# Kernel tuning notes

Hardware: AMD Instinct MI355X
Metric: run time of the kernel (lower is better)

Reference implementation:

```python
import jax, jax.numpy as jnp
import numpy as np

B, D, E, C = 16384, 768, 124, 6  # batch, emb_dim, n_experts, n_classes


def _mlp(h, w1, b1, w2, b2):
    # timm Mlp: fc1 -> GELU(exact) -> fc2, hidden = in_features
    return jax.nn.gelu(h @ w1 + b1, approximate=False) @ w2 + b2


def setup_inputs() -> dict:
    key = jax.random.key(0)
    ks = jax.random.split(key, 14)
    s = 0.02
    inp = {
        "x": jax.random.normal(ks[0], (B, D), dtype=jnp.float32),
        # per-sample expert counts in [1, E]
        "n_experts": jax.random.randint(ks[1], (B,), 1, E + 1, dtype=jnp.int64 if jax.config.jax_enable_x64 else jnp.int32),
        # classifier Mlp: D -> D -> E*C
        "cls_w1": jax.random.normal(ks[2], (D, D), dtype=jnp.float32) * s,
        "cls_b1": jnp.zeros((D,), jnp.float32),
        "cls_w2": jax.random.normal(ks[3], (D, E * C), dtype=jnp.float32) * s,
        "cls_b2": jnp.zeros((E * C,), jnp.float32),
        # which_expert Mlp: D -> D -> E
        "we_w1": jax.random.normal(ks[4], (D, D), dtype=jnp.float32) * s,
        "we_b1": jnp.zeros((D,), jnp.float32),
        "we_w2": jax.random.normal(ks[5], (D, E), dtype=jnp.float32) * s,
        "we_b2": jnp.zeros((E,), jnp.float32),
        # expert_weights Mlp: D -> D -> E
        "ew_w1": jax.random.normal(ks[6], (D, D), dtype=jnp.float32) * s,
        "ew_b1": jnp.zeros((D,), jnp.float32),
        "ew_w2": jax.random.normal(ks[7], (D, E), dtype=jnp.float32) * s,
        "ew_b2": jnp.zeros((E,), jnp.float32),
    }
    return inp


def reference(x, n_experts, cls_w1, cls_b1, cls_w2, cls_b2,
              we_w1, we_b1, we_w2, we_b2, ew_w1, ew_b1, ew_w2, ew_b2):
    emb = x  # backbone = identity
    expert_logits = _mlp(emb, cls_w1, cls_b1, cls_w2, cls_b2).reshape(B, E, C)
    expert_weight_logits = _mlp(emb, ew_w1, ew_b1, ew_w2, ew_b2)  # [B, E]
    which_expert = _mlp(emb, we_w1, we_b1, we_w2, we_b2)          # [B, E]

    n = jnp.minimum(n_experts, E)                                  # clamp to n_experts
    # kth_largest: sort descending, pick (n-1)-th per row -> threshold
    sorted_desc = -jnp.sort(-which_expert, axis=1)
    threshold = sorted_desc[jnp.arange(B), n - 1][:, None]         # [B, 1]
    mask = which_expert < threshold

    expert_weight_logits = jnp.where(mask, -jnp.inf, expert_weight_logits)
    expert_proba = jax.nn.softmax(expert_logits, axis=2)           # over classes
    expert_weights = jax.nn.softmax(expert_weight_logits, axis=1)  # over experts

    combined = (expert_proba * expert_weights[:, :, None]).sum(axis=1)
    return combined / expert_weights.sum(axis=1)[:, None]          # [B, C]
```

## Files before the change

kernel.cpp:

```cpp
#include <hip/hip_runtime.h>
#include <stdint.h>

typedef unsigned short u16;
typedef short short8 __attribute__((ext_vector_type(8)));
typedef float f32x4 __attribute__((ext_vector_type(4)));

#define NB 16384

#define OFF_XHI      0ull
#define OFF_XLO      25165824ull
#define OFF_LCLS     0ull
#define OFF_LWE_P0   25165824ull
#define OFF_LWE_P1   33554432ull
#define OFF_LWE_P2   41943040ull
#define OFF_BT1      50331648ull
#define OFF_LEWB     50331648ull
#define OFF_BTWE_HI  52690944ull
#define OFF_BTWE_LO  53870592ull
#define OFF_BT2CLS   55050240ull
#define OFF_BT2EW    56229888ull
#define OFF_BT2WE_HI 56426496ull
#define OFF_BT2WE_LO 56623104ull
#define OFF_B1CE     56819712ull
#define OFF_B1WE     56825856ull
#define OFF_B2CLS    56828928ull
#define OFF_B2EW     56832000ull
#define OFF_B2WE     56832512ull
#define OFF_HCLSEW   56833024ull
#define OFF_HWE_HI   107164672ull
#define OFF_HWE_LO   132330496ull
#define WS_NEED      157496320ull

__device__ __forceinline__ u16 f2bf(float f) {
  uint32_t u = __float_as_uint(f);
  u += 0x7fffu + ((u >> 16) & 1u);
  return (u16)(u >> 16);
}
__device__ __forceinline__ float bf2f(u16 h) {
  return __uint_as_float(((uint32_t)h) << 16);
}
__device__ __forceinline__ void g2l16(const u16* g, u16* l) {
  __builtin_amdgcn_global_load_lds(
      (__attribute__((address_space(1))) void*)(u16*)g,
      (__attribute__((address_space(3))) void*)l, 16, 0, 0);
}

__global__ void prep_all(
    const float* __restrict__ x, u16* __restrict__ xhi, u16* __restrict__ xlo,
    const float* __restrict__ cls_w1, const float* __restrict__ ew_w1,
    const float* __restrict__ we_w1,  const float* __restrict__ cls_w2,
    const float* __restrict__ ew_w2,  const float* __restrict__ we_w2,
    u16* BT1, u16* BTwe_hi, u16* BTwe_lo,
    u16* BT2cls, u16* BT2ew, u16* BT2we_hi, u16* BT2we_lo,
    const float* __restrict__ cls_b1, const float* __restrict__ ew_b1,
    const float* __restrict__ we_b1,  const float* __restrict__ cls_b2,
    const float* __restrict__ ew_b2,  const float* __restrict__ we_b2,
    float* b1ce, float* b1we, float* b2cls, float* b2ew, float* b2we) {
  __shared__ float t[64][65];
  const int bid = blockIdx.x;
  if (bid < 12288) {
    int i = bid * 256 + threadIdx.x;
    float4 v = ((const float4*)x)[i];
    ushort4 h, l;
    h.x = f2bf(v.x); l.x = f2bf(v.x - bf2f(h.x));
    h.y = f2bf(v.y); l.y = f2bf(v.y - bf2f(h.y));
    h.z = f2bf(v.z); l.z = f2bf(v.z - bf2f(h.z));
    h.w = f2bf(v.w); l.w = f2bf(v.w - bf2f(h.w));
    ((ushort4*)xhi)[i] = h;
    ((ushort4*)xlo)[i] = l;
    return;
  }
  if (bid < 13152) {
    const int idx = bid - 12288;
    const int bx = idx % 12, by = (idx / 12) % 12, bz = idx / 144;
    const float* src; int N; u16* dhi; u16* dlo = nullptr;
    switch (bz) {
      case 0: src = cls_w1; N = 768; dhi = BT1; break;
      case 1: src = ew_w1;  N = 768; dhi = BT1 + 768 * 768; break;
      case 2: src = we_w1;  N = 768; dhi = BTwe_hi; dlo = BTwe_lo; break;
      case 3: src = cls_w2; N = 744; dhi = BT2cls; break;
      case 4: src = ew_w2;  N = 124; dhi = BT2ew; break;
      default: src = we_w2; N = 124; dhi = BT2we_hi; dlo = BT2we_lo; break;
    }
    const int Npad = (N + 127) & ~127;
    const int n0 = by * 64;
    if (n0 >= Npad) return;
    const int k0 = bx * 64;
    const int tx = threadIdx.x & 63, tg = threadIdx.x >> 6;
#pragma unroll
    for (int r = 0; r < 16; ++r) {
      int k = tg * 16 + r;
      int n = n0 + tx;
      t[k][tx] = (n < N) ? src[(size_t)(k0 + k) * N + n] : 0.f;
    }
    __syncthreads();
#pragma unroll
    for (int r = 0; r < 16; ++r) {
      int n = n0 + tg * 16 + r;
      if (n < Npad) {
        float v = t[tx][tg * 16 + r];
        u16 h = f2bf(v);
        dhi[(size_t)n * 768 + k0 + tx] = h;
        if (dlo) dlo[(size_t)n * 768 + k0 + tx] = f2bf(v - bf2f(h));
      }
    }
    return;
  }
  int id = (bid - 13152) * 256 + threadIdx.x;
  if (id < 1536) { b1ce[id] = (id < 768) ? cls_b1[id] : ew_b1[id - 768]; return; }
  id -= 1536;
  if (id < 768) { b1we[id] = we_b1[id]; return; }
  id -= 768;
  if (id < 768) { b2cls[id] = (id < 744) ? cls_b2[id] : 0.f; return; }
  id -= 768;
  if (id < 128) { b2ew[id] = (id < 124) ? ew_b2[id] : 0.f; return; }
  id -= 128;
  if (id < 128) { b2we[id] = (id < 124) ? we_b2[id] : 0.f; return; }
}

__device__ __forceinline__ void gemm_core(
    const u16* A0, const u16* A1, const u16* A2, int lda,
    const u16* B0, const u16* B1, const u16* B2,
    int npass, int K, int bm, int tid, u16* sA, u16* sB, f32x4 acc[4][4]) {
  const int lane = tid & 63;
  const int wv = tid >> 6;
  const int wr = wv >> 1, wc = wv & 1;
  const int sr = lane >> 3;
  const int sc = (((lane & 7) ^ sr) << 3);
  for (int p = 0; p < npass; ++p) {
    const u16* A = (p == 0) ? A0 : ((p == 1) ? A1 : A2);
    const u16* Bp = (p == 0) ? B0 : ((p == 1) ? B1 : B2);
    const u16* gA = A + (size_t)(bm + wv * 32 + sr) * lda + sc;
    const u16* gB = Bp + (size_t)(wv * 32 + sr) * K + sc;
    u16* lA = sA + (wv * 32) * 64;
    u16* lB = sB + (wv * 32) * 64;
    for (int kt = 0; kt < K; kt += 64) {
#pragma unroll
      for (int s = 0; s < 4; ++s) {
        g2l16(gA + (size_t)(s * 8) * lda + kt, lA + s * 8 * 64);
        g2l16(gB + (size_t)(s * 8) * K + kt, lB + s * 8 * 64);
      }
      __syncthreads();
#pragma unroll
      for (int ks = 0; ks < 2; ++ks) {
        const int co = ((ks * 4 + (lane >> 4)) ^ (lane & 7)) * 8;
        short8 av[4], bv[4];
#pragma unroll
        for (int i = 0; i < 4; i++)
          av[i] = *(const short8*)(sA + (wr * 64 + i * 16 + (lane & 15)) * 64 + co);
#pragma unroll
        for (int j = 0; j < 4; j++)
          bv[j] = *(const short8*)(sB + (wc * 64 + j * 16 + (lane & 15)) * 64 + co);
#pragma unroll
        for (int i = 0; i < 4; i++)
#pragma unroll
          for (int j = 0; j < 4; j++)
            acc[i][j] = __builtin_amdgcn_mfma_f32_16x16x32_bf16(av[i], bv[j], acc[i][j], 0, 0, 0);
      }
      __syncthreads();
    }
  }
}

__device__ __forceinline__ void gemm_split_core(
    const u16* __restrict__ Ahi, const u16* __restrict__ Alo, int lda,
    const u16* __restrict__ Bhi, const u16* __restrict__ Blo, int ldb,
    int K, int bm, int tid, u16* sA, u16* sB, f32x4 acc[4][4]) {
  const int lane = tid & 63;
  const int wv = tid >> 6;
  const int wr = wv >> 1, wc = wv & 1;
  const int sr = lane >> 3;
  const int gl = (lane & 7) ^ sr;
  const int koff = (gl & 3) << 3;
  const u16* Asel = (gl < 4) ? Ahi : Alo;
  const u16* Bsel = (gl < 4) ? Bhi : Blo;
  const u16* gA = Asel + (size_t)(bm + wv * 32 + sr) * lda + koff;
  const u16* gB = Bsel + (size_t)(wv * 32 + sr) * ldb + koff;
  u16* lA = sA + (wv * 32) * 64;
  u16* lB = sB + (wv * 32) * 64;

  for (int kt = 0; kt < K; kt += 32) {
#pragma unroll
    for (int s = 0; s < 4; ++s) {
      g2l16(gA + (size_t)(s * 8) * lda + kt, lA + s * 8 * 64);
      g2l16(gB + (size_t)(s * 8) * ldb + kt, lB + s * 8 * 64);
    }
    __syncthreads();
    const int coh = (((lane >> 4) ^ (lane & 7)) << 3);
    short8 ah[4], al[4], bh[4], bl[4];
#pragma unroll
    for (int i = 0; i < 4; i++) {
      const u16* p = sA + (wr * 64 + i * 16 + (lane & 15)) * 64;
      ah[i] = *(const short8*)(p + coh);
      al[i] = *(const short8*)(p + (coh ^ 32));
    }
#pragma unroll
    for (int j = 0; j < 4; j++) {
      const u16* p = sB + (wc * 64 + j * 16 + (lane & 15)) * 64;
      bh[j] = *(const short8*)(p + coh);
      bl[j] = *(const short8*)(p + (coh ^ 32));
    }
#pragma unroll
    for (int i = 0; i < 4; i++)
#pragma unroll
      for (int j = 0; j < 4; j++) {
        acc[i][j] = __builtin_amdgcn_mfma_f32_16x16x32_bf16(ah[i], bh[j], acc[i][j], 0, 0, 0);
        acc[i][j] = __builtin_amdgcn_mfma_f32_16x16x32_bf16(al[i], bh[j], acc[i][j], 0, 0, 0);
        acc[i][j] = __builtin_amdgcn_mfma_f32_16x16x32_bf16(ah[i], bl[j], acc[i][j], 0, 0, 0);
      }
    __syncthreads();
  }
}

__device__ __forceinline__ void decode_bid(int bid, int NC, int& bm, int& bn) {
  const int xcd = bid & 7, slot = bid >> 3;
  const int per = NC << 3;
  const int sub = slot / per, rem = slot - sub * per;
  const int colu = rem >> 3, rowIn = rem & 7;
  bm = ((xcd << 4) + (sub << 3) + rowIn) << 7;
  bn = colu << 7;
}

__global__ __launch_bounds__(256, 4) void gemm1_fused(
    const u16* __restrict__ Ahi, const u16* __restrict__ Alo,
    const u16* __restrict__ Bwe_hi, const u16* __restrict__ Bwe_lo,
    const u16* __restrict__ BT1,
    const float* __restrict__ b1we, const float* __restrict__ b1ce,
    u16* __restrict__ out_we_hi, u16* __restrict__ out_we_lo,
    u16* __restrict__ out_ce) {
  __shared__ u16 smem[2 * 128 * 64];
  u16* sA = smem;
  u16* sB = smem + 128 * 64;
  const int tid = threadIdx.x;
  const int lane = tid & 63;
  const int wr = (tid >> 6) >> 1, wc = (tid >> 6) & 1;
  const int K = 768;

  f32x4 acc[4][4];
#pragma unroll
  for (int i = 0; i < 4; i++)
#pragma unroll
    for (int j = 0; j < 4; j++) acc[i][j] = f32x4{0.f, 0.f, 0.f, 0.f};

  if (blockIdx.x < 768) {
    int bm, bn;
    decode_bid(blockIdx.x, 6, bm, bn);
    gemm_split_core(Ahi, Alo, K, Bwe_hi + (size_t)bn * K, Bwe_lo + (size_t)bn * K, K,
                    K, bm, tid, sA, sB, acc);
#pragma unroll
    for (int j = 0; j < 4; j++) {
      const int col = bn + wc * 64 + j * 16 + (lane & 15);
      const float bs = b1we[col];
#pragma unroll
      for (int i = 0; i < 4; i++) {
        const int row0 = bm + wr * 64 + i * 16 + (lane >> 4) * 4;
#pragma unroll
        for (int r = 0; r < 4; r++) {
          float v = acc[i][j][r] + bs;
          const size_t idx = (size_t)(row0 + r) * 768 + col;
          float g = 0.5f * v * (1.0f + erff(v * 0.70710678118654752f));
          u16 h = f2bf(g);
          out_we_hi[idx] = h;
          out_we_lo[idx] = f2bf(g - bf2f(h));
        }
      }
    }
  } else {
    int bm, bn;
    decode_bid(blockIdx.x - 768, 12, bm, bn);
    gemm_core(Ahi, nullptr, nullptr, 768, BT1 + (size_t)bn * K, nullptr, nullptr,
              1, K, bm, tid, sA, sB, acc);
#pragma unroll
    for (int j = 0; j < 4; j++) {
      const int col = bn + wc * 64 + j * 16 + (lane & 15);
      const float bs = b1ce[col];
#pragma unroll
      for (int i = 0; i < 4; i++) {
        const int row0 = bm + wr * 64 + i * 16 + (lane >> 4) * 4;
#pragma unroll
        for (int r = 0; r < 4; r++) {
          float v = acc[i][j][r] + bs;
          float g = 0.5f * v * (1.0f + erff(v * 0.70710678118654752f));
          out_ce[(size_t)(row0 + r) * 1536 + col] = f2bf(g);
        }
      }
    }
  }
}

__global__ __launch_bounds__(256, 4) void gemm2_fused(
    const u16* __restrict__ h_cls,
    const u16* __restrict__ hwe_hi, const u16* __restrict__ hwe_lo,
    const u16* __restrict__ BT2cls, const u16* __restrict__ BT2ew,
    const u16* __restrict__ BT2we_hi, const u16* __restrict__ BT2we_lo,
    const float* __restrict__ b2cls, const float* __restrict__ b2ew,
    const float* __restrict__ b2we,
    u16* __restrict__ Lcls, u16* __restrict__ LewB,
    float* __restrict__ p0, float* __restrict__ p1, float* __restrict__ p2) {
  __shared__ u16 sA[128 * 64];
  __shared__ u16 sB[128 * 64];
  const int tid = threadIdx.x;
  const int lane = tid & 63;
  const int wr = (tid >> 6) >> 1, wc = (tid >> 6) & 1;

  f32x4 acc[4][4];
#pragma unroll
  for (int i = 0; i < 4; i++)
#pragma unroll
    for (int j = 0; j < 4; j++) acc[i][j] = f32x4{0.f, 0.f, 0.f, 0.f};

  const int bid = blockIdx.x;
  if (bid < 768) {
    int bm, bn;
    decode_bid(bid, 6, bm, bn);
    gemm_core(h_cls, nullptr, nullptr, 1536, BT2cls + (size_t)bn * 768, nullptr, nullptr,
              1, 768, bm, tid, sA, sB, acc);
#pragma unroll
    for (int j = 0; j < 4; j++) {
      const int col = bn + wc * 64 + j * 16 + (lane & 15);
      const float bs = b2cls[col];
#pragma unroll
      for (int i = 0; i < 4; i++) {
        const int row0 = bm + wr * 64 + i * 16 + (lane >> 4) * 4;
#pragma unroll
        for (int r = 0; r < 4; r++)
          Lcls[(size_t)(row0 + r) * 768 + col] = f2bf(acc[i][j][r] + bs);
      }
    }
  } else if (bid < 896) {
    const int r = bid - 768;
    const int bm = (((r & 7) << 4) + (r >> 3)) << 7;
    gemm_core(h_cls + 768, nullptr, nullptr, 1536, BT2ew, nullptr, nullptr,
              1, 768, bm, tid, sA, sB, acc);
#pragma unroll
    for (int j = 0; j < 4; j++) {
      const int col = wc * 64 + j * 16 + (lane & 15);
      const float bs = b2ew[col];
#pragma unroll
      for (int i = 0; i < 4; i++) {
        const int row0 = bm + wr * 64 + i * 16 + (lane >> 4) * 4;
#pragma unroll
        for (int r2 = 0; r2 < 4; r2++)
          LewB[(size_t)(row0 + r2) * 128 + col] = f2bf(acc[i][j][r2] + bs);
      }
    }
  } else {
    const int q = bid - 896;
    const int pass = q >> 7;
    const int r = q & 127;
    const int bm = (((r & 7) << 4) + (r >> 3)) << 7;
    const u16* A = (pass == 1) ? hwe_lo : hwe_hi;
    const u16* Bp = (pass == 2) ? BT2we_lo : BT2we_hi;
    gemm_core(A, nullptr, nullptr, 768, Bp, nullptr, nullptr,
              1, 768, bm, tid, sA, sB, acc);
    float* o = (pass == 0) ? p0 : ((pass == 1) ? p1 : p2);
#pragma unroll
    for (int j = 0; j < 4; j++) {
      const int col = wc * 64 + j * 16 + (lane & 15);
      const float bs = (pass == 0) ? b2we[col] : 0.f;
#pragma unroll
      for (int i = 0; i < 4; i++) {
        const int row0 = bm + wr * 64 + i * 16 + (lane >> 4) * 4;
#pragma unroll
        for (int r2 = 0; r2 < 4; r2++)
          o[(size_t)(row0 + r2) * 128 + col] = acc[i][j][r2] + bs;
      }
    }
  }
}

__global__ __launch_bounds__(256) void finalize(
    const u16* __restrict__ Lcls,
    const float* __restrict__ p0, const float* __restrict__ p1,
    const float* __restrict__ p2,
    const u16* __restrict__ LewB,
    const int* __restrict__ nexp, float* __restrict__ out) {
  const int bid = blockIdx.x;
  const int g = ((bid & 7) << 9) + (bid >> 3);
  const int b = (g << 2) + (int)(threadIdx.x >> 6);
  const int lane = threadIdx.x & 63;
  const float NEG = -3.0e38f;
  const size_t base = (size_t)b * 128;
  const float w0 = (lane < 124) ? (p0[base + lane] + p1[base + lane] + p2[base + lane]) : NEG;
  const float w1 = (lane < 60) ? (p0[base + 64 + lane] + p1[base + 64 + lane] + p2[base + 64 + lane]) : NEG;
  int r0 = 0, r1 = 0;
#pragma unroll
  for (int j = 0; j < 64; ++j) {
    float v = __shfl(w0, j, 64);
    r0 += (v > w0); r1 += (v > w1);
  }
#pragma unroll
  for (int j = 0; j < 64; ++j) {
    float v = __shfl(w1, j, 64);
    r0 += (v > w0); r1 += (v > w1);
  }
  int n = nexp[b];
  n = n < 1 ? 1 : (n > 124 ? 124 : n);
  const bool k0 = (lane < 124) && (r0 < n);
  const bool k1 = (lane < 60) && (r1 < n);
  float l0 = k0 ? bf2f(LewB[base + lane]) : NEG;
  float l1 = k1 ? bf2f(LewB[base + 64 + lane]) : NEG;
  float mx = fmaxf(l0, l1);
#pragma unroll
  for (int o = 32; o > 0; o >>= 1) mx = fmaxf(mx, __shfl_xor(mx, o, 64));
  float e0 = k0 ? __expf(l0 - mx) : 0.f;
  float e1 = k1 ? __expf(l1 - mx) : 0.f;
  float S = e0 + e1;
#pragma unroll
  for (int o = 32; o > 0; o >>= 1) S += __shfl_xor(S, o, 64);
  float a0 = 0, a1 = 0, a2 = 0, a3 = 0, a4 = 0, a5 = 0;
#pragma unroll
  for (int h = 0; h < 2; ++h) {
    int e = lane + h * 64;
    float we = h ? e1 : e0;
    if (we > 0.f) {
      const u16* lp = Lcls + (size_t)b * 768 + e * 6;
      float c0 = bf2f(lp[0]), c1 = bf2f(lp[1]), c2 = bf2f(lp[2]);
      float c3 = bf2f(lp[3]), c4 = bf2f(lp[4]), c5 = bf2f(lp[5]);
      float m = fmaxf(fmaxf(fmaxf(c0, c1), fmaxf(c2, c3)), fmaxf(c4, c5));
      float q0 = __expf(c0 - m), q1 = __expf(c1 - m), q2 = __expf(c2 - m);
      float q3 = __expf(c3 - m), q4 = __expf(c4 - m), q5 = __expf(c5 - m);
      float inv = we / (q0 + q1 + q2 + q3 + q4 + q5);
      a0 += q0 * inv; a1 += q1 * inv; a2 += q2 * inv;
      a3 += q3 * inv; a4 += q4 * inv; a5 += q5 * inv;
    }
  }
#pragma unroll
  for (int o = 32; o > 0; o >>= 1) {
    a0 += __shfl_xor(a0, o, 64); a1 += __shfl_xor(a1, o, 64);
    a2 += __shfl_xor(a2, o, 64); a3 += __shfl_xor(a3, o, 64);
    a4 += __shfl_xor(a4, o, 64); a5 += __shfl_xor(a5, o, 64);
  }
  if (lane < 6) {
    float v = (lane == 0) ? a0 : (lane == 1) ? a1 : (lane == 2) ? a2
              : (lane == 3) ? a3 : (lane == 4) ? a4 : a5;
    out[(size_t)b * 6 + lane] = v / S;
  }
}

__global__ void fill_sentinel(float* out, int n, float v) {
  int i = blockIdx.x * 256 + threadIdx.x;
  if (i < n) out[i] = v;
}

extern "C" void kernel_launch(void* const* d_in, const int* in_sizes, int n_in,
                              void* d_out, int out_size, void* d_ws, size_t ws_size,
                              hipStream_t stream) {
  const float* x = (const float*)d_in[0];
  const int* nexp = (const int*)d_in[1];
  const float* cls_w1 = (const float*)d_in[2];
  const float* cls_b1 = (const float*)d_in[3];
  const float* cls_w2 = (const float*)d_in[4];
  const float* cls_b2 = (const float*)d_in[5];
  const float* we_w1 = (const float*)d_in[6];
  const float* we_b1 = (const float*)d_in[7];
  const float* we_w2 = (const float*)d_in[8];
  const float* we_b2 = (const float*)d_in[9];
  const float* ew_w1 = (const float*)d_in[10];
  const float* ew_b1 = (const float*)d_in[11];
  const float* ew_w2 = (const float*)d_in[12];
  const float* ew_b2 = (const float*)d_in[13];
  float* out = (float*)d_out;
  char* ws = (char*)d_ws;

  if (ws_size < WS_NEED) {
    fill_sentinel<<<(out_size + 255) / 256, 256, 0, stream>>>(out, out_size, 12345.0f);
    return;
  }

  u16* xhi = (u16*)(ws + OFF_XHI);
  u16* xlo = (u16*)(ws + OFF_XLO);
  u16* Lcls = (u16*)(ws + OFF_LCLS);
  float* pwe0 = (float*)(ws + OFF_LWE_P0);
  float* pwe1 = (float*)(ws + OFF_LWE_P1);
  float* pwe2 = (float*)(ws + OFF_LWE_P2);
  u16* LewB = (u16*)(ws + OFF_LEWB);
  u16* BT1 = (u16*)(ws + OFF_BT1);
  u16* BTwe_hi = (u16*)(ws + OFF_BTWE_HI);
  u16* BTwe_lo = (u16*)(ws + OFF_BTWE_LO);
  u16* BT2cls = (u16*)(ws + OFF_BT2CLS);
  u16* BT2ew = (u16*)(ws + OFF_BT2EW);
  u16* BT2we_hi = (u16*)(ws + OFF_BT2WE_HI);
  u16* BT2we_lo = (u16*)(ws + OFF_BT2WE_LO);
  float* b1ce = (float*)(ws + OFF_B1CE);
  float* b1we = (float*)(ws + OFF_B1WE);
  float* b2cls = (float*)(ws + OFF_B2CLS);
  float* b2ew = (float*)(ws + OFF_B2EW);
  float* b2we = (float*)(ws + OFF_B2WE);
  u16* h_clsew = (u16*)(ws + OFF_HCLSEW);
  u16* h_we_hi = (u16*)(ws + OFF_HWE_HI);
  u16* h_we_lo = (u16*)(ws + OFF_HWE_LO);

  prep_all<<<13165, 256, 0, stream>>>(x, xhi, xlo,
                                      cls_w1, ew_w1, we_w1, cls_w2, ew_w2, we_w2,
                                      BT1, BTwe_hi, BTwe_lo, BT2cls, BT2ew, BT2we_hi, BT2we_lo,
                                      cls_b1, ew_b1, we_b1, cls_b2, ew_b2, we_b2,
                                      b1ce, b1we, b2cls, b2ew, b2we);
  gemm1_fused<<<2304, 256, 0, stream>>>(xhi, xlo, BTwe_hi, BTwe_lo, BT1,
                                        b1we, b1ce, h_we_hi, h_we_lo, h_clsew);
  gemm2_fused<<<1280, 256, 0, stream>>>(h_clsew, h_we_hi, h_we_lo,
                                        BT2cls, BT2ew, BT2we_hi, BT2we_lo,
                                        b2cls, b2ew, b2we,
                                        Lcls, LewB, pwe0, pwe1, pwe2);
  finalize<<<4096, 256, 0, stream>>>(Lcls, pwe0, pwe1, pwe2, LewB, nexp, out);
}
```

Baseline: 345.3 us.

## Use 256x256 double-buffered 8-wave GEMM tiles with polynomial GELU and merged split passes

Replaces the 128x128, 4-wave GEMM cores with a templated 256x256 tile on 512-thread blocks. K-tiles are double-buffered in LDS, half-tiles are staged while quarter-tiles of MFMA run, and s_setprio is raised around the MFMA blocks. Exact erff in the GELU epilogue is replaced by an Abramowitz-Stegun polynomial with a fast exp. The which_expert second GEMM now treats the hi and lo weight halves as one 256-wide B, which drops the third partial buffer and the matching load in finalize. The aim is more data reuse per tile and less load latency and epilogue cost, at the price of higher register and LDS pressure, fewer blocks, and a slightly different erf approximation.

Result: slower. 378.0 us (+9.5%).

```diff
diff --git a/kernel.cpp b/kernel.cpp
--- a/kernel.cpp
+++ b/kernel.cpp
@@ -5,14 +5,12 @@
 typedef short short8 __attribute__((ext_vector_type(8)));
 typedef float f32x4 __attribute__((ext_vector_type(4)));
 
-#define NB 16384
 
 #define OFF_XHI      0ull
 #define OFF_XLO      25165824ull
 #define OFF_LCLS     0ull
 #define OFF_LWE_P0   25165824ull
 #define OFF_LWE_P1   33554432ull
-#define OFF_LWE_P2   41943040ull
 #define OFF_BT1      50331648ull
 #define OFF_LEWB     50331648ull
 #define OFF_BTWE_HI  52690944ull
@@ -43,6 +41,20 @@
   __builtin_amdgcn_global_load_lds(
       (__attribute__((address_space(1))) void*)(u16*)g,
       (__attribute__((address_space(3))) void*)l, 16, 0, 0);
+}
+
+__device__ __forceinline__ float gelu_exact(float v) {
+  const float x = fabsf(v) * 0.70710678118654752f;
+  const float t = __fdividef(1.0f, __builtin_fmaf(0.3275911f, x, 1.0f));
+  float p = __builtin_fmaf(1.061405429f, t, -1.453152027f);
+  p = __builtin_fmaf(p, t, 1.421413741f);
+  p = __builtin_fmaf(p, t, -0.284496736f);
+  p = __builtin_fmaf(p, t, 0.254829592f);
+  p = p * t;
+  const float e = __expf(-x * x);
+  float erfx = __builtin_fmaf(-p, e, 1.0f);
+  erfx = (v < 0.f) ? -erfx : erfx;
+  return 0.5f * v * (1.0f + erfx);
 }
 
 __global__ void prep_all(
@@ -118,147 +130,205 @@
   if (id < 128) { b2we[id] = (id < 124) ? we_b2[id] : 0.f; return; }
 }
 
-__device__ __forceinline__ void gemm_core(
+
+__device__ __forceinline__ void stage_half(const u16* gsrc, int ld, u16* smem,
+                                           int bufsel, int isB, int h,
+                                           int wv, int srow, int scol) {
+  const int rb = isB ? (h << 7) : (h << 6);
+  const int rs = isB ? 64 : 128;
+  u16* lb = smem + bufsel * 32768 + isB * 16384 + (rb + (wv << 3)) * 64;
+  const u16* gs = gsrc + (size_t)(rb + (wv << 3) + srow) * ld + scol;
+  g2l16(gs, lb);
+  g2l16(gs + (size_t)rs * ld, lb + rs * 64);
+}
+
+__device__ __forceinline__ void rd_a(const u16* base, int wr, int lane, int mh,
+                                     short8 a[4][2]) {
+  const int r0 = wr * 128 + mh * 64 + (lane & 15);
+  const int g0 = lane >> 4;
+#pragma unroll
+  for (int i = 0; i < 4; ++i)
+#pragma unroll
+    for (int ks = 0; ks < 2; ++ks) {
+      const int pg = (ks * 4 + g0) ^ (lane & 7);
+      a[i][ks] = *(const short8*)(base + (size_t)(r0 + i * 16) * 64 + pg * 8);
+    }
+}
+__device__ __forceinline__ void rd_b(const u16* base, int wc, int lane, int nh,
+                                     short8 b[2][2]) {
+  const int r0 = wc * 64 + nh * 32 + (lane & 15);
+  const int g0 = lane >> 4;
+#pragma unroll
+  for (int j = 0; j < 2; ++j)
+#pragma unroll
+    for (int ks = 0; ks < 2; ++ks) {
+      const int pg = (ks * 4 + g0) ^ (lane & 7);
+      b[j][ks] = *(const short8*)(base + (size_t)(r0 + j * 16) * 64 + pg * 8);
+    }
+}
+
+#define PH_WAIT()                                          \
+  __builtin_amdgcn_s_barrier();                            \
+  asm volatile("s_waitcnt lgkmcnt(0)" ::: "memory");       \
+  __builtin_amdgcn_sched_barrier(0);
+
+template <int NPASS>
+__device__ __forceinline__ void gemm256_core(
     const u16* A0, const u16* A1, const u16* A2, int lda,
-    const u16* B0, const u16* B1, const u16* B2,
-    int npass, int K, int bm, int tid, u16* sA, u16* sB, f32x4 acc[4][4]) {
+    const u16* B0, const u16* B1, const u16* B2, int ldb,
+    int ktpp, int tid, u16* smem, f32x4 acc[8][4]) {
   const int lane = tid & 63;
   const int wv = tid >> 6;
-  const int wr = wv >> 1, wc = wv & 1;
-  const int sr = lane >> 3;
-  const int sc = (((lane & 7) ^ sr) << 3);
-  for (int p = 0; p < npass; ++p) {
-    const u16* A = (p == 0) ? A0 : ((p == 1) ? A1 : A2);
-    const u16* Bp = (p == 0) ? B0 : ((p == 1) ? B1 : B2);
-    const u16* gA = A + (size_t)(bm + wv * 32 + sr) * lda + sc;
-    const u16* gB = Bp + (size_t)(wv * 32 + sr) * K + sc;
-    u16* lA = sA + (wv * 32) * 64;
-    u16* lB = sB + (wv * 32) * 64;
-    for (int kt = 0; kt < K; kt += 64) {
-#pragma unroll
-      for (int s = 0; s < 4; ++s) {
-        g2l16(gA + (size_t)(s * 8) * lda + kt, lA + s * 8 * 64);
-        g2l16(gB + (size_t)(s * 8) * K + kt, lB + s * 8 * 64);
-      }
-      __syncthreads();
-#pragma unroll
-      for (int ks = 0; ks < 2; ++ks) {
-        const int co = ((ks * 4 + (lane >> 4)) ^ (lane & 7)) * 8;
-        short8 av[4], bv[4];
-#pragma unroll
-        for (int i = 0; i < 4; i++)
-          av[i] = *(const short8*)(sA + (wr * 64 + i * 16 + (lane & 15)) * 64 + co);
-#pragma unroll
-        for (int j = 0; j < 4; j++)
-          bv[j] = *(const short8*)(sB + (wc * 64 + j * 16 + (lane & 15)) * 64 + co);
-#pragma unroll
-        for (int i = 0; i < 4; i++)
-#pragma unroll
-          for (int j = 0; j < 4; j++)
-            acc[i][j] = __builtin_amdgcn_mfma_f32_16x16x32_bf16(av[i], bv[j], acc[i][j], 0, 0, 0);
-      }
-      __syncthreads();
-    }
-  }
-}
-
-__device__ __forceinline__ void gemm_split_core(
-    const u16* __restrict__ Ahi, const u16* __restrict__ Alo, int lda,
-    const u16* __restrict__ Bhi, const u16* __restrict__ Blo, int ldb,
-    int K, int bm, int tid, u16* sA, u16* sB, f32x4 acc[4][4]) {
-  const int lane = tid & 63;
-  const int wv = tid >> 6;
-  const int wr = wv >> 1, wc = wv & 1;
-  const int sr = lane >> 3;
-  const int gl = (lane & 7) ^ sr;
-  const int koff = (gl & 3) << 3;
-  const u16* Asel = (gl < 4) ? Ahi : Alo;
-  const u16* Bsel = (gl < 4) ? Bhi : Blo;
-  const u16* gA = Asel + (size_t)(bm + wv * 32 + sr) * lda + koff;
-  const u16* gB = Bsel + (size_t)(wv * 32 + sr) * ldb + koff;
-  u16* lA = sA + (wv * 32) * 64;
-  u16* lB = sB + (wv * 32) * 64;
-
-  for (int kt = 0; kt < K; kt += 32) {
-#pragma unroll
-    for (int s = 0; s < 4; ++s) {
-      g2l16(gA + (size_t)(s * 8) * lda + kt, lA + s * 8 * 64);
-      g2l16(gB + (size_t)(s * 8) * ldb + kt, lB + s * 8 * 64);
-    }
-    __syncthreads();
-    const int coh = (((lane >> 4) ^ (lane & 7)) << 3);
-    short8 ah[4], al[4], bh[4], bl[4];
-#pragma unroll
-    for (int i = 0; i < 4; i++) {
-      const u16* p = sA + (wr * 64 + i * 16 + (lane & 15)) * 64;
-      ah[i] = *(const short8*)(p + coh);
-      al[i] = *(const short8*)(p + (coh ^ 32));
-    }
-#pragma unroll
-    for (int j = 0; j < 4; j++) {
-      const u16* p = sB + (wc * 64 + j * 16 + (lane & 15)) * 64;
-      bh[j] = *(const short8*)(p + coh);
-      bl[j] = *(const short8*)(p + (coh ^ 32));
-    }
-#pragma unroll
-    for (int i = 0; i < 4; i++)
-#pragma unroll
-      for (int j = 0; j < 4; j++) {
-        acc[i][j] = __builtin_amdgcn_mfma_f32_16x16x32_bf16(ah[i], bh[j], acc[i][j], 0, 0, 0);
-        acc[i][j] = __builtin_amdgcn_mfma_f32_16x16x32_bf16(al[i], bh[j], acc[i][j], 0, 0, 0);
-        acc[i][j] = __builtin_amdgcn_mfma_f32_16x16x32_bf16(ah[i], bl[j], acc[i][j], 0, 0, 0);
-      }
-    __syncthreads();
-  }
-}
-
-__device__ __forceinline__ void decode_bid(int bid, int NC, int& bm, int& bn) {
+  const int wr = wv >> 2, wc = wv & 3;
+  const int srow = lane >> 3;
+  const int scol = ((lane & 7) ^ srow) << 3;
+  const int NT = NPASS * ktpp;
+
+  auto aP = [&](int nt) -> const u16* {
+    int p = 0, kk = nt;
+    if (NPASS > 1 && kk >= ktpp) { kk -= ktpp; ++p; }
+    if (NPASS > 2 && kk >= ktpp) { kk -= ktpp; ++p; }
+    const u16* base = (p == 0) ? A0 : ((p == 1) ? A1 : A2);
+    return base + kk * 64;
+  };
+  auto bP = [&](int nt) -> const u16* {
+    int p = 0, kk = nt;
+    if (NPASS > 1 && kk >= ktpp) { kk -= ktpp; ++p; }
+    if (NPASS > 2 && kk >= ktpp) { kk -= ktpp; ++p; }
+    const u16* base = (p == 0) ? B0 : ((p == 1) ? B1 : B2);
+    return base + kk * 64;
+  };
+  auto mmaQ = [&](int mh, int nh, short8 (&av)[4][2], short8 (&bv)[2][2]) {
+    __builtin_amdgcn_s_setprio(1);
+#pragma unroll
+    for (int i = 0; i < 4; ++i)
+#pragma unroll
+      for (int j = 0; j < 2; ++j)
+#pragma unroll
+        for (int ks = 0; ks < 2; ++ks)
+          acc[mh * 4 + i][nh * 2 + j] = __builtin_amdgcn_mfma_f32_16x16x32_bf16(
+              av[i][ks], bv[j][ks], acc[mh * 4 + i][nh * 2 + j], 0, 0, 0);
+    __builtin_amdgcn_s_setprio(0);
+  };
+
+  {
+    const u16* a0p = aP(0); const u16* b0p = bP(0);
+    const u16* a1p = aP(1); const u16* b1p = bP(1);
+    stage_half(a0p, lda, smem, 0, 0, 0, wv, srow, scol);
+    stage_half(b0p, ldb, smem, 0, 1, 1, wv, srow, scol);
+    stage_half(a0p, lda, smem, 0, 0, 1, wv, srow, scol);
+    stage_half(b0p, ldb, smem, 0, 1, 0, wv, srow, scol);
+    stage_half(a1p, lda, smem, 1, 0, 0, wv, srow, scol);
+    stage_half(b1p, ldb, smem, 1, 1, 1, wv, srow, scol);
+    stage_half(a1p, lda, smem, 1, 0, 1, wv, srow, scol);
+  }
+  asm volatile("s_waitcnt vmcnt(6)" ::: "memory");
+  __builtin_amdgcn_s_barrier();
+
+  const u16* sA0 = smem;
+  const u16* sB0 = smem + 16384;
+  const u16* sA1 = smem + 32768;
+  const u16* sB1 = smem + 32768 + 16384;
+
+  short8 a[4][2], b0v[2][2], b1v[2][2];
+
+  for (int t = 0; t < NT; t += 2) {
+    const bool more = (t + 2 < NT);
+    const u16* a2p = more ? aP(t + 2) : A0;
+    const u16* b2p = more ? bP(t + 2) : B0;
+    const u16* a3p = more ? aP(t + 3) : A0;
+    const u16* b3p = more ? bP(t + 3) : B0;
+    const u16* b1p_ = bP(t + 1);
+
+    stage_half(b1p_, ldb, smem, 1, 1, 0, wv, srow, scol);
+    rd_a(sA0, wr, lane, 0, a);
+    rd_b(sB0, wc, lane, 0, b0v);
+    PH_WAIT();
+    mmaQ(0, 0, a, b0v);
+    __builtin_amdgcn_s_barrier();
+    if (more) stage_half(a2p, lda, smem, 0, 0, 0, wv, srow, scol);
+    rd_b(sB0, wc, lane, 1, b1v);
+    PH_WAIT();
+    mmaQ(0, 1, a, b1v);
+    __builtin_amdgcn_s_barrier();
+    if (more) stage_half(b2p, ldb, smem, 0, 1, 1, wv, srow, scol);
+    rd_a(sA0, wr, lane, 1, a);
+    PH_WAIT();
+    mmaQ(1, 1, a, b1v);
+    __builtin_amdgcn_s_barrier();
+    if (more) stage_half(a2p, lda, smem, 0, 0, 1, wv, srow, scol);
+    __builtin_amdgcn_s_barrier();
+    mmaQ(1, 0, a, b0v);
+    if (more) asm volatile("s_waitcnt vmcnt(6)" ::: "memory");
+    else      asm volatile("s_waitcnt vmcnt(0)" ::: "memory");
+    __builtin_amdgcn_s_barrier();
+    if (more) stage_half(b2p, ldb, smem, 0, 1, 0, wv, srow, scol);
+    rd_a(sA1, wr, lane, 0, a);
+    rd_b(sB1, wc, lane, 0, b0v);
+    PH_WAIT();
+    mmaQ(0, 0, a, b0v);
+    __builtin_amdgcn_s_barrier();
+    if (more) stage_half(a3p, lda, smem, 1, 0, 0, wv, srow, scol);
+    rd_b(sB1, wc, lane, 1, b1v);
+    PH_WAIT();
+    mmaQ(0, 1, a, b1v);
+    __builtin_amdgcn_s_barrier();
+    if (more) stage_half(b3p, ldb, smem, 1, 1, 1, wv, srow, scol);
+    rd_a(sA1, wr, lane, 1, a);
+    PH_WAIT();
+    mmaQ(1, 1, a, b1v);
+    __builtin_amdgcn_s_barrier();
+    if (more) stage_half(a3p, lda, smem, 1, 0, 1, wv, srow, scol);
+    __builtin_amdgcn_s_barrier();
+    mmaQ(1, 0, a, b0v);
+    if (more) asm volatile("s_waitcnt vmcnt(6)" ::: "memory");
+    __builtin_amdgcn_s_barrier();
+  }
+}
+
+__device__ __forceinline__ void decode256(int bid, int& bm, int& bn) {
   const int xcd = bid & 7, slot = bid >> 3;
-  const int per = NC << 3;
-  const int sub = slot / per, rem = slot - sub * per;
-  const int colu = rem >> 3, rowIn = rem & 7;
-  bm = ((xcd << 4) + (sub << 3) + rowIn) << 7;
-  bn = colu << 7;
-}
-
-__global__ __launch_bounds__(256, 4) void gemm1_fused(
+  bm = ((xcd << 3) + (slot & 7)) << 8;
+  bn = (slot >> 3) << 8;
+}
+
+__global__ __launch_bounds__(512, 2) void gemm1_fused(
     const u16* __restrict__ Ahi, const u16* __restrict__ Alo,
     const u16* __restrict__ Bwe_hi, const u16* __restrict__ Bwe_lo,
     const u16* __restrict__ BT1,
     const float* __restrict__ b1we, const float* __restrict__ b1ce,
     u16* __restrict__ out_we_hi, u16* __restrict__ out_we_lo,
     u16* __restrict__ out_ce) {
-  __shared__ u16 smem[2 * 128 * 64];
-  u16* sA = smem;
-  u16* sB = smem + 128 * 64;
+  __shared__ u16 smem[65536];
   const int tid = threadIdx.x;
   const int lane = tid & 63;
-  const int wr = (tid >> 6) >> 1, wc = (tid >> 6) & 1;
-  const int K = 768;
-
-  f32x4 acc[4][4];
-#pragma unroll
-  for (int i = 0; i < 4; i++)
+  const int wv = tid >> 6;
+  const int wr = wv >> 2, wc = wv & 3;
+  f32x4 acc[8][4];
+#pragma unroll
+  for (int i = 0; i < 8; i++)
 #pragma unroll
     for (int j = 0; j < 4; j++) acc[i][j] = f32x4{0.f, 0.f, 0.f, 0.f};
 
-  if (blockIdx.x < 768) {
+  if (blockIdx.x < 192) {
     int bm, bn;
-    decode_bid(blockIdx.x, 6, bm, bn);
-    gemm_split_core(Ahi, Alo, K, Bwe_hi + (size_t)bn * K, Bwe_lo + (size_t)bn * K, K,
-                    K, bm, tid, sA, sB, acc);
+    decode256(blockIdx.x, bm, bn);
+    gemm256_core<3>(Ahi + (size_t)bm * 768, Alo + (size_t)bm * 768,
+                    Ahi + (size_t)bm * 768, 768,
+                    Bwe_hi + (size_t)bn * 768, Bwe_hi + (size_t)bn * 768,
+                    Bwe_lo + (size_t)bn * 768, 768,
+                    12, tid, smem, acc);
 #pragma unroll
     for (int j = 0; j < 4; j++) {
-      const int col = bn + wc * 64 + j * 16 + (lane & 15);
+      const int col = bn + wc * 64 + ((j >> 1) << 5) + ((j & 1) << 4) + (lane & 15);
       const float bs = b1we[col];
 #pragma unroll
-      for (int i = 0; i < 4; i++) {
-        const int row0 = bm + wr * 64 + i * 16 + (lane >> 4) * 4;
+      for (int i = 0; i < 8; i++) {
+        const int row0 = bm + wr * 128 + ((i >> 2) << 6) + ((i & 3) << 4) + ((lane >> 4) << 2);
 #pragma unroll
         for (int r = 0; r < 4; r++) {
-          float v = acc[i][j][r] + bs;
+          float g = gelu_exact(acc[i][j][r] + bs);
           const size_t idx = (size_t)(row0 + r) * 768 + col;
-          float g = 0.5f * v * (1.0f + erff(v * 0.70710678118654752f));
           u16 h = f2bf(g);
           out_we_hi[idx] = h;
           out_we_lo[idx] = f2bf(g - bf2f(h));
@@ -267,20 +337,20 @@
     }
   } else {
     int bm, bn;
-    decode_bid(blockIdx.x - 768, 12, bm, bn);
-    gemm_core(Ahi, nullptr, nullptr, 768, BT1 + (size_t)bn * K, nullptr, nullptr,
-              1, K, bm, tid, sA, sB, acc);
+    decode256(blockIdx.x - 192, bm, bn);
+    gemm256_core<1>(Ahi + (size_t)bm * 768, nullptr, nullptr, 768,
+                    BT1 + (size_t)bn * 768, nullptr, nullptr, 768,
+                    12, tid, smem, acc);
 #pragma unroll
     for (int j = 0; j < 4; j++) {
-      const int col = bn + wc * 64 + j * 16 + (lane & 15);
+      const int col = bn + wc * 64 + ((j >> 1) << 5) + ((j & 1) << 4) + (lane & 15);
       const float bs = b1ce[col];
 #pragma unroll
-      for (int i = 0; i < 4; i++) {
-        const int row0 = bm + wr * 64 + i * 16 + (lane >> 4) * 4;
+      for (int i = 0; i < 8; i++) {
+        const int row0 = bm + wr * 128 + ((i >> 2) << 6) + ((i & 3) << 4) + ((lane >> 4) << 2);
 #pragma unroll
         for (int r = 0; r < 4; r++) {
-          float v = acc[i][j][r] + bs;
-          float g = 0.5f * v * (1.0f + erff(v * 0.70710678118654752f));
+          float g = gelu_exact(acc[i][j][r] + bs);
           out_ce[(size_t)(row0 + r) * 1536 + col] = f2bf(g);
         }
       }
@@ -288,92 +358,88 @@
   }
 }
 
-__global__ __launch_bounds__(256, 4) void gemm2_fused(
-    const u16* __restrict__ h_cls,
-    const u16* __restrict__ hwe_hi, const u16* __restrict__ hwe_lo,
-    const u16* __restrict__ BT2cls, const u16* __restrict__ BT2ew,
-    const u16* __restrict__ BT2we_hi, const u16* __restrict__ BT2we_lo,
+__global__ __launch_bounds__(512, 2) void gemm2_fused(
+    const u16* __restrict__ h_cls, const u16* __restrict__ hwe_hi,
+    const u16* __restrict__ hwe_lo, const u16* __restrict__ BT2cls,
+    const u16* __restrict__ BT2ew, const u16* __restrict__ BT2we,
     const float* __restrict__ b2cls, const float* __restrict__ b2ew,
     const float* __restrict__ b2we,
     u16* __restrict__ Lcls, u16* __restrict__ LewB,
-    float* __restrict__ p0, float* __restrict__ p1, float* __restrict__ p2) {
-  __shared__ u16 sA[128 * 64];
-  __shared__ u16 sB[128 * 64];
+    float* __restrict__ p0, float* __restrict__ p1) {
+  __shared__ u16 smem[65536];
   const int tid = threadIdx.x;
   const int lane = tid & 63;
-  const int wr = (tid >> 6) >> 1, wc = (tid >> 6) & 1;
-
-  f32x4 acc[4][4];
-#pragma unroll
-  for (int i = 0; i < 4; i++)
+  const int wv = tid >> 6;
+  const int wr = wv >> 2, wc = wv & 3;
+  f32x4 acc[8][4];
+#pragma unroll
+  for (int i = 0; i < 8; i++)
 #pragma unroll
     for (int j = 0; j < 4; j++) acc[i][j] = f32x4{0.f, 0.f, 0.f, 0.f};
 
   const int bid = blockIdx.x;
-  if (bid < 768) {
+  if (bid < 64) {
+    const int bm = (((bid & 7) << 3) + (bid >> 3)) << 8;
+    gemm256_core<2>(hwe_hi + (size_t)bm * 768, hwe_lo + (size_t)bm * 768, nullptr, 768,
+                    BT2we, BT2we, nullptr, 768, 12, tid, smem, acc);
+    const int inlo = wc >> 1;
+    float* o = inlo ? p1 : p0;
+    const int cb = (wc & 1) * 64;
+#pragma unroll
+    for (int j = 0; j < 4; j++) {
+      const int col = cb + ((j >> 1) << 5) + ((j & 1) << 4) + (lane & 15);
+      const float bs = inlo ? 0.f : b2we[col];
+#pragma unroll
+      for (int i = 0; i < 8; i++) {
+        const int row0 = bm + wr * 128 + ((i >> 2) << 6) + ((i & 3) << 4) + ((lane >> 4) << 2);
+#pragma unroll
+        for (int r = 0; r < 4; r++)
+          o[(size_t)(row0 + r) * 128 + col] = acc[i][j][r] + bs;
+      }
+    }
+  } else if (bid < 128) {
+    const int q = bid - 64;
+    const int bm = (((q & 7) << 3) + (q >> 3)) << 8;
+    gemm256_core<1>(h_cls + 768 + (size_t)bm * 1536, nullptr, nullptr, 1536,
+                    BT2ew, nullptr, nullptr, 768, 12, tid, smem, acc);
+    if (wc < 2) {
+#pragma unroll
+      for (int j = 0; j < 4; j++) {
+        const int col = wc * 64 + ((j >> 1) << 5) + ((j & 1) << 4) + (lane & 15);
+        const float bs = b2ew[col];
+#pragma unroll
+        for (int i = 0; i < 8; i++) {
+          const int row0 = bm + wr * 128 + ((i >> 2) << 6) + ((i & 3) << 4) + ((lane >> 4) << 2);
+#pragma unroll
+          for (int r = 0; r < 4; r++)
+            LewB[(size_t)(row0 + r) * 128 + col] = f2bf(acc[i][j][r] + bs);
+        }
+      }
+    }
+  } else {
     int bm, bn;
-    decode_bid(bid, 6, bm, bn);
-    gemm_core(h_cls, nullptr, nullptr, 1536, BT2cls + (size_t)bn * 768, nullptr, nullptr,
-              1, 768, bm, tid, sA, sB, acc);
+    decode256(bid - 128, bm, bn);
+    gemm256_core<1>(h_cls + (size_t)bm * 1536, nullptr, nullptr, 1536,
+                    BT2cls + (size_t)bn * 768, nullptr, nullptr, 768,
+                    12, tid, smem, acc);
 #pragma unroll
     for (int j = 0; j < 4; j++) {
-      const int col = bn + wc * 64 + j * 16 + (lane & 15);
+      const int col = bn + wc * 64 + ((j >> 1) << 5) + ((j & 1) << 4) + (lane & 15);
       const float bs = b2cls[col];
 #pragma unroll
-      for (int i = 0; i < 4; i++) {
-        const int row0 = bm + wr * 64 + i * 16 + (lane >> 4) * 4;
+      for (int i = 0; i < 8; i++) {
+        const int row0 = bm + wr * 128 + ((i >> 2) << 6) + ((i & 3) << 4) + ((lane >> 4) << 2);
 #pragma unroll
         for (int r = 0; r < 4; r++)
           Lcls[(size_t)(row0 + r) * 768 + col] = f2bf(acc[i][j][r] + bs);
       }
     }
-  } else if (bid < 896) {
-    const int r = bid - 768;
-    const int bm = (((r & 7) << 4) + (r >> 3)) << 7;
-    gemm_core(h_cls + 768, nullptr, nullptr, 1536, BT2ew, nullptr, nullptr,
-              1, 768, bm, tid, sA, sB, acc);
-#pragma unroll
-    for (int j = 0; j < 4; j++) {
-      const int col = wc * 64 + j * 16 + (lane & 15);
-      const float bs = b2ew[col];
-#pragma unroll
-      for (int i = 0; i < 4; i++) {
-        const int row0 = bm + wr * 64 + i * 16 + (lane >> 4) * 4;
-#pragma unroll
-        for (int r2 = 0; r2 < 4; r2++)
-          LewB[(size_t)(row0 + r2) * 128 + col] = f2bf(acc[i][j][r2] + bs);
-      }
-    }
-  } else {
-    const int q = bid - 896;
-    const int pass = q >> 7;
-    const int r = q & 127;
-    const int bm = (((r & 7) << 4) + (r >> 3)) << 7;
-    const u16* A = (pass == 1) ? hwe_lo : hwe_hi;
-    const u16* Bp = (pass == 2) ? BT2we_lo : BT2we_hi;
-    gemm_core(A, nullptr, nullptr, 768, Bp, nullptr, nullptr,
-              1, 768, bm, tid, sA, sB, acc);
-    float* o = (pass == 0) ? p0 : ((pass == 1) ? p1 : p2);
-#pragma unroll
-    for (int j = 0; j < 4; j++) {
-      const int col = wc * 64 + j * 16 + (lane & 15);
-      const float bs = (pass == 0) ? b2we[col] : 0.f;
-#pragma unroll
-      for (int i = 0; i < 4; i++) {
-        const int row0 = bm + wr * 64 + i * 16 + (lane >> 4) * 4;
-#pragma unroll
-        for (int r2 = 0; r2 < 4; r2++)
-          o[(size_t)(row0 + r2) * 128 + col] = acc[i][j][r2] + bs;
-      }
-    }
   }
 }
 
 __global__ __launch_bounds__(256) void finalize(
-    const u16* __restrict__ Lcls,
-    const float* __restrict__ p0, const float* __restrict__ p1,
-    const float* __restrict__ p2,
-    const u16* __restrict__ LewB,
+    const u16* __restrict__ Lcls, const float* __restrict__ p0,
+    const float* __restrict__ p1, const u16* __restrict__ LewB,
     const int* __restrict__ nexp, float* __restrict__ out) {
   const int bid = blockIdx.x;
   const int g = ((bid & 7) << 9) + (bid >> 3);
@@ -381,8 +447,8 @@
   const int lane = threadIdx.x & 63;
   const float NEG = -3.0e38f;
   const size_t base = (size_t)b * 128;
-  const float w0 = (lane < 124) ? (p0[base + lane] + p1[base + lane] + p2[base + lane]) : NEG;
-  const float w1 = (lane < 60) ? (p0[base + 64 + lane] + p1[base + 64 + lane] + p2[base + 64 + lane]) : NEG;
+  const float w0 = (lane < 124) ? (p0[base + lane] + p1[base + lane]) : NEG;
+  const float w1 = (lane < 60) ? (p0[base + 64 + lane] + p1[base + 64 + lane]) : NEG;
   int r0 = 0, r1 = 0;
 #pragma unroll
   for (int j = 0; j < 64; ++j) {
@@ -473,7 +539,6 @@
   u16* Lcls = (u16*)(ws + OFF_LCLS);
   float* pwe0 = (float*)(ws + OFF_LWE_P0);
   float* pwe1 = (float*)(ws + OFF_LWE_P1);
-  float* pwe2 = (float*)(ws + OFF_LWE_P2);
   u16* LewB = (u16*)(ws + OFF_LEWB);
   u16* BT1 = (u16*)(ws + OFF_BT1);
   u16* BTwe_hi = (u16*)(ws + OFF_BTWE_HI);
@@ -496,11 +561,11 @@
                                       BT1, BTwe_hi, BTwe_lo, BT2cls, BT2ew, BT2we_hi, BT2we_lo,
                                       cls_b1, ew_b1, we_b1, cls_b2, ew_b2, we_b2,
                                       b1ce, b1we, b2cls, b2ew, b2we);
-  gemm1_fused<<<2304, 256, 0, stream>>>(xhi, xlo, BTwe_hi, BTwe_lo, BT1,
-                                        b1we, b1ce, h_we_hi, h_we_lo, h_clsew);
-  gemm2_fused<<<1280, 256, 0, stream>>>(h_clsew, h_we_hi, h_we_lo,
-                                        BT2cls, BT2ew, BT2we_hi, BT2we_lo,
-                                        b2cls, b2ew, b2we,
-                                        Lcls, LewB, pwe0, pwe1, pwe2);
-  finalize<<<4096, 256, 0, stream>>>(Lcls, pwe0, pwe1, pwe2, LewB, nexp, out);
-}
+  gemm1_fused<<<576, 512, 0, stream>>>(xhi, xlo, BTwe_hi, BTwe_lo, BT1,
+                                       b1we, b1ce, h_we_hi, h_we_lo, h_clsew);
+  gemm2_fused<<<320, 512, 0, stream>>>(h_clsew, h_we_hi, h_we_lo,
+                                       BT2cls, BT2ew, BT2we_hi,
+                                       b2cls, b2ew, b2we,
+                                       Lcls, LewB, pwe0, pwe1);
+  finalize<<<4096, 256, 0, stream>>>(Lcls, pwe0, pwe1, LewB, nexp, out);
+}
```

## Split-K the which-expert layer-2 GEMM and use polynomial erf in GELU

Applied to the files above, without the earlier changes.

The which-expert second GEMM previously ran as three separate pass GEMMs (hi*hi, lo*hi, hi*lo), each writing its own fp32 partial buffer. It now uses the fused split-precision core over two K halves, writing two partials, so gemm2 has fewer blocks and finalize reads one less buffer. The GELU epilogue in gemm1 replaces erff with an Abramowitz-Stegun polynomial built on fast exp and fast divide. That polynomial has about 1e-7 absolute error, which could slightly perturb the top-k expert selection near ties.

Result: no change. 351.2 us (+1.7%).

```diff
diff --git a/kernel.cpp b/kernel.cpp
--- a/kernel.cpp
+++ b/kernel.cpp
@@ -12,7 +12,6 @@
 #define OFF_LCLS     0ull
 #define OFF_LWE_P0   25165824ull
 #define OFF_LWE_P1   33554432ull
-#define OFF_LWE_P2   41943040ull
 #define OFF_BT1      50331648ull
 #define OFF_LEWB     50331648ull
 #define OFF_BTWE_HI  52690944ull
@@ -43,6 +42,20 @@
   __builtin_amdgcn_global_load_lds(
       (__attribute__((address_space(1))) void*)(u16*)g,
       (__attribute__((address_space(3))) void*)l, 16, 0, 0);
+}
+
+__device__ __forceinline__ float gelu_exact(float v) {
+  const float x = fabsf(v) * 0.70710678118654752f;
+  const float t = __fdividef(1.0f, __builtin_fmaf(0.3275911f, x, 1.0f));
+  float p = __builtin_fmaf(1.061405429f, t, -1.453152027f);
+  p = __builtin_fmaf(p, t, 1.421413741f);
+  p = __builtin_fmaf(p, t, -0.284496736f);
+  p = __builtin_fmaf(p, t, 0.254829592f);
+  p = p * t;
+  const float e = __expf(-x * x);
+  float erfx = __builtin_fmaf(-p, e, 1.0f);
+  erfx = (v < 0.f) ? -erfx : erfx;
+  return 0.5f * v * (1.0f + erfx);
 }
 
 __global__ void prep_all(
@@ -256,9 +269,8 @@
         const int row0 = bm + wr * 64 + i * 16 + (lane >> 4) * 4;
 #pragma unroll
         for (int r = 0; r < 4; r++) {
-          float v = acc[i][j][r] + bs;
+          float g = gelu_exact(acc[i][j][r] + bs);
           const size_t idx = (size_t)(row0 + r) * 768 + col;
-          float g = 0.5f * v * (1.0f + erff(v * 0.70710678118654752f));
           u16 h = f2bf(g);
           out_we_hi[idx] = h;
           out_we_lo[idx] = f2bf(g - bf2f(h));
@@ -279,8 +291,7 @@
         const int row0 = bm + wr * 64 + i * 16 + (lane >> 4) * 4;
 #pragma unroll
         for (int r = 0; r < 4; r++) {
-          float v = acc[i][j][r] + bs;
-          float g = 0.5f * v * (1.0f + erff(v * 0.70710678118654752f));
+          float g = gelu_exact(acc[i][j][r] + bs);
           out_ce[(size_t)(row0 + r) * 1536 + col] = f2bf(g);
         }
       }
@@ -296,7 +307,7 @@
     const float* __restrict__ b2cls, const float* __restrict__ b2ew,
     const float* __restrict__ b2we,
     u16* __restrict__ Lcls, u16* __restrict__ LewB,
-    float* __restrict__ p0, float* __restrict__ p1, float* __restrict__ p2) {
+    float* __restrict__ p0, float* __restrict__ p1) {
   __shared__ u16 sA[128 * 64];
   __shared__ u16 sB[128 * 64];
   const int tid = threadIdx.x;
@@ -310,9 +321,30 @@
     for (int j = 0; j < 4; j++) acc[i][j] = f32x4{0.f, 0.f, 0.f, 0.f};
 
   const int bid = blockIdx.x;
-  if (bid < 768) {
+  if (bid < 256) {
+    const int half = bid >> 7;
+    const int r = bid & 127;
+    const int bm = (((r & 7) << 4) + (r >> 3)) << 7;
+    const int k0 = half * 384;
+    gemm_split_core(hwe_hi + k0, hwe_lo + k0, 768,
+                    BT2we_hi + k0, BT2we_lo + k0, 768,
+                    384, bm, tid, sA, sB, acc);
+    float* o = half ? p1 : p0;
+#pragma unroll
+    for (int j = 0; j < 4; j++) {
+      const int col = wc * 64 + j * 16 + (lane & 15);
+      const float bs = half ? 0.f : b2we[col];
+#pragma unroll
+      for (int i = 0; i < 4; i++) {
+        const int row0 = bm + wr * 64 + i * 16 + (lane >> 4) * 4;
+#pragma unroll
+        for (int r2 = 0; r2 < 4; r2++)
+          o[(size_t)(row0 + r2) * 128 + col] = acc[i][j][r2] + bs;
+      }
+    }
+  } else if (bid < 1024) {
     int bm, bn;
-    decode_bid(bid, 6, bm, bn);
+    decode_bid(bid - 256, 6, bm, bn);
     gemm_core(h_cls, nullptr, nullptr, 1536, BT2cls + (size_t)bn * 768, nullptr, nullptr,
               1, 768, bm, tid, sA, sB, acc);
 #pragma unroll
@@ -327,8 +359,8 @@
           Lcls[(size_t)(row0 + r) * 768 + col] = f2bf(acc[i][j][r] + bs);
       }
     }
-  } else if (bid < 896) {
-    const int r = bid - 768;
+  } else {
+    const int r = bid - 1024;
     const int bm = (((r & 7) << 4) + (r >> 3)) << 7;
     gemm_core(h_cls + 768, nullptr, nullptr, 1536, BT2ew, nullptr, nullptr,
               1, 768, bm, tid, sA, sB, acc);
@@ -344,35 +376,12 @@
           LewB[(size_t)(row0 + r2) * 128 + col] = f2bf(acc[i][j][r2] + bs);
       }
     }
-  } else {
-    const int q = bid - 896;
-    const int pass = q >> 7;
-    const int r = q & 127;
-    const int bm = (((r & 7) << 4) + (r >> 3)) << 7;
-    const u16* A = (pass == 1) ? hwe_lo : hwe_hi;
-    const u16* Bp = (pass == 2) ? BT2we_lo : BT2we_hi;
-    gemm_core(A, nullptr, nullptr, 768, Bp, nullptr, nullptr,
-              1, 768, bm, tid, sA, sB, acc);
-    float* o = (pass == 0) ? p0 : ((pass == 1) ? p1 : p2);
-#pragma unroll
-    for (int j = 0; j < 4; j++) {
-      const int col = wc * 64 + j * 16 + (lane & 15);
-      const float bs = (pass == 0) ? b2we[col] : 0.f;
-#pragma unroll
-      for (int i = 0; i < 4; i++) {
-        const int row0 = bm + wr * 64 + i * 16 + (lane >> 4) * 4;
-#pragma unroll
-        for (int r2 = 0; r2 < 4; r2++)
-          o[(size_t)(row0 + r2) * 128 + col] = acc[i][j][r2] + bs;
-      }
-    }
   }
 }
 
 __global__ __launch_bounds__(256) void finalize(
     const u16* __restrict__ Lcls,
     const float* __restrict__ p0, const float* __restrict__ p1,
-    const float* __restrict__ p2,
     const u16* __restrict__ LewB,
     const int* __restrict__ nexp, float* __restrict__ out) {
   const int bid = blockIdx.x;
@@ -381,8 +390,8 @@
   const int lane = threadIdx.x & 63;
   const float NEG = -3.0e38f;
   const size_t base = (size_t)b * 128;
-  const float w0 = (lane < 124) ? (p0[base + lane] + p1[base + lane] + p2[base + lane]) : NEG;
-  const float w1 = (lane < 60) ? (p0[base + 64 + lane] + p1[base + 64 + lane] + p2[base + 64 + lane]) : NEG;
+  const float w0 = (lane < 124) ? (p0[base + lane] + p1[base + lane]) : NEG;
+  const float w1 = (lane < 60) ? (p0[base + 64 + lane] + p1[base + 64 + lane]) : NEG;
   int r0 = 0, r1 = 0;
 #pragma unroll
   for (int j = 0; j < 64; ++j) {
@@ -473,7 +482,6 @@
   u16* Lcls = (u16*)(ws + OFF_LCLS);
   float* pwe0 = (float*)(ws + OFF_LWE_P0);
   float* pwe1 = (float*)(ws + OFF_LWE_P1);
-  float* pwe2 = (float*)(ws + OFF_LWE_P2);
   u16* LewB = (u16*)(ws + OFF_LEWB);
   u16* BT1 = (u16*)(ws + OFF_BT1);
   u16* BTwe_hi = (u16*)(ws + OFF_BTWE_HI);
@@ -498,9 +506,9 @@
                                       b1ce, b1we, b2cls, b2ew, b2we);
   gemm1_fused<<<2304, 256, 0, stream>>>(xhi, xlo, BTwe_hi, BTwe_lo, BT1,
                                         b1we, b1ce, h_we_hi, h_we_lo, h_clsew);
-  gemm2_fused<<<1280, 256, 0, stream>>>(h_clsew, h_we_hi, h_we_lo,
+  gemm2_fused<<<1152, 256, 0, stream>>>(h_clsew, h_we_hi, h_we_lo,
                                         BT2cls, BT2ew, BT2we_hi, BT2we_lo,
                                         b2cls, b2ew, b2we,
-                                        Lcls, LewB, pwe0, pwe1, pwe2);
-  finalize<<<4096, 256, 0, stream>>>(Lcls, pwe0, pwe1, pwe2, LewB, nexp, out);
-}
+                                        Lcls, LewB, pwe0, pwe1);
+  finalize<<<4096, 256, 0, stream>>>(Lcls, pwe0, pwe1, LewB, nexp, out);
+}
```
